# Kernel optimization log

Hardware: AMD Instinct MI355X
Metric: run time of the kernel (lower is better)

## Reference

```python
import jax, jax.numpy as jnp
import numpy as np
from jax import lax

BN_EPS = 1e-5


def _spatial_gate(x, w, g, b, m, v):
    # x: [N, C, H, W]; ChannelPool -> [N, 2, H, W]; 7x7 conv -> [N,1,H,W]; BN (eval); sigmoid gate
    comp = jnp.stack([jnp.max(x, axis=1), jnp.mean(x, axis=1)], axis=1)
    o = lax.conv_general_dilated(comp, w, (1, 1), [(3, 3), (3, 3)],
                                 dimension_numbers=('NCHW', 'OIHW', 'NCHW'))
    o = (o - m[None, :, None, None]) * lax.rsqrt(v + BN_EPS)[None, :, None, None] \
        * g[None, :, None, None] + b[None, :, None, None]
    s = jax.nn.sigmoid(o)
    return x * s


def _eca_sort(x, w_eca):
    # global avg pool -> sort channels desc -> 1D conv over sorted seq -> sigmoid -> unsort -> gate
    y = jnp.mean(x, axis=(2, 3))               # [N, C]
    order = jnp.argsort(-y, axis=1)            # descending sort indices
    rank = jnp.argsort(order, axis=1)          # inverse permutation
    ys = jnp.take_along_axis(y, order, axis=1)  # sorted descending
    k = w_eca.shape[-1]
    p = k // 2
    o = lax.conv_general_dilated(ys[:, None, :], w_eca, (1,), [(p, p)],
                                 dimension_numbers=('NCH', 'OIH', 'NCH'))[:, 0, :]
    sig = jax.nn.sigmoid(o)
    yr = jnp.take_along_axis(sig, rank, axis=1)  # reorder back per original index_select(rank)
    return x * yr[:, :, None, None]


def setup_inputs() -> dict:
    key = jax.random.key(0)
    ks = jax.random.split(key, 6)
    N, C, H, W = 32, 256, 56, 56
    inp = {
        'x': jax.random.normal(ks[0], (N, C, H, W), dtype=jnp.float32),
        'weight': jax.random.normal(ks[1], (1,), dtype=jnp.float32),
        'w_h': jax.random.normal(ks[2], (1, 2, 7, 7), dtype=jnp.float32) * 0.1,
        'g_h': jnp.ones((1,), jnp.float32), 'b_h': jnp.zeros((1,), jnp.float32),
        'm_h': jnp.zeros((1,), jnp.float32), 'v_h': jnp.ones((1,), jnp.float32),
        'w_w': jax.random.normal(ks[3], (1, 2, 7, 7), dtype=jnp.float32) * 0.1,
        'g_w': jnp.ones((1,), jnp.float32), 'b_w': jnp.zeros((1,), jnp.float32),
        'm_w': jnp.zeros((1,), jnp.float32), 'v_w': jnp.ones((1,), jnp.float32),
        'w_s': jax.random.normal(ks[4], (1, 2, 7, 7), dtype=jnp.float32) * 0.1,
        'g_s': jnp.ones((1,), jnp.float32), 'b_s': jnp.zeros((1,), jnp.float32),
        'm_s': jnp.zeros((1,), jnp.float32), 'v_s': jnp.ones((1,), jnp.float32),
        'w_eca': jax.random.normal(ks[5], (1, 1, 5), dtype=jnp.float32) * 0.3,
    }
    return inp


def reference(x, weight, w_h, g_h, b_h, m_h, v_h, w_w, g_w, b_w, m_w, v_w,
              w_s, g_s, b_s, m_s, v_s, w_eca):
    # branch 1: gate over H-as-channel (permute 0,2,1,3)
    xh = jnp.transpose(x, (0, 2, 1, 3))
    x11 = jnp.transpose(_spatial_gate(xh, w_h, g_h, b_h, m_h, v_h), (0, 2, 1, 3))
    # branch 2: gate over W-as-channel (permute 0,3,2,1)
    xw = jnp.transpose(x, (0, 3, 2, 1))
    x21 = jnp.transpose(_spatial_gate(xw, w_w, g_w, b_w, m_w, v_w), (0, 3, 2, 1))
    # branch 3: eca with sort/unsort
    x31 = _eca_sort(x, w_eca)
    # branch 4: plain spatial gate
    xo = _spatial_gate(x, w_s, g_s, b_s, m_s, v_s)
    return 0.23779 * xo + 0.24695 * x11 + 0.24365 * x21 + 0.27173 * x31
```

## Files before the change

### kernel.cpp

```cpp
#include <hip/hip_runtime.h>
#include <math.h>

#define N_ 32
#define C_ 256
#define H_ 56
#define W_ 56
#define HW_ (H_*W_)
#define HW4_ (HW_/4)
#define CHW_ (C_*HW_)
#define NHW_ (N_*HW_)
#define NCW_ (N_*C_*W_)
#define NHC_ (N_*H_*C_)
#define BN_EPS_ 1e-5f

#define TLD 60
#define PLANES_PER_BLK 8
#define NB_PL 1024
#define NB_CP 784

#define SM_BUF1 3360
#define SM_CPMX 6720
#define SM_CPSM (6720 + 224)
#define SM_TOT  (6720 + 448)

__global__ __launch_bounds__(256) void pools_k(
        const float* __restrict__ x,
        float* __restrict__ maxC, float* __restrict__ meanC,
        float* __restrict__ maxH, float* __restrict__ meanH,
        float* __restrict__ maxW, float* __restrict__ meanW,
        float* __restrict__ y) {
    __shared__ float smem[SM_TOT];
    int b = blockIdx.x;
    int tid = threadIdx.x;
    const float4* x4 = (const float4*)x;
    if (b < NB_PL) {
        float* buf0 = smem;
        float* buf1 = smem + SM_BUF1;
        float* cpmx = smem + SM_CPMX;
        float* cpsm = smem + SM_CPSM;
        int pb0 = b * PLANES_PER_BLK;
        float4 r0, r1, r2, r3;
        int row0 = tid / 14,          col0 = (tid % 14) * 4;
        int row1 = (tid + 256) / 14,  col1 = ((tid + 256) % 14) * 4;
        int row2 = (tid + 512) / 14,  col2 = ((tid + 512) % 14) * 4;
        int row3 = (tid + 768) / 14,  col3 = ((tid + 768) % 14) * 4;
        {
            size_t base = (size_t)pb0 * HW4_;
            r0 = x4[base + tid];
            r1 = x4[base + 256 + tid];
            r2 = x4[base + 512 + tid];
            if (tid < 16) r3 = x4[base + 768 + tid];
        }
        {
            float* d = buf0;
            *(float4*)&d[row0 * TLD + col0] = r0;
            *(float4*)&d[row1 * TLD + col1] = r1;
            *(float4*)&d[row2 * TLD + col2] = r2;
            if (tid < 16) *(float4*)&d[row3 * TLD + col3] = r3;
        }
        __syncthreads();
        for (int k = 0; k < PLANES_PER_BLK; ++k) {
            float* cur = (k & 1) ? buf1 : buf0;
            float* nxt = (k & 1) ? buf0 : buf1;
            int pb = pb0 + k;
            int n = pb >> 8, c = pb & 255;
            if (k < PLANES_PER_BLK - 1) {
                size_t base = (size_t)(pb + 1) * HW4_;
                r0 = x4[base + tid];
                r1 = x4[base + 256 + tid];
                r2 = x4[base + 512 + tid];
                if (tid < 16) r3 = x4[base + 768 + tid];
            }
            if (tid < 224) {
                int w = tid % 56, hq = tid / 56;
                const float* base = &cur[(hq * 14) * TLD + w];
                float mx = -INFINITY, sm = 0.f;
                #pragma unroll
                for (int hh = 0; hh < 14; ++hh) {
                    float v = base[hh * TLD];
                    mx = fmaxf(mx, v); sm += v;
                }
                cpmx[hq * 56 + w] = mx;
                cpsm[hq * 56 + w] = sm;
            }
            __syncthreads();
            float colsum = 0.f;
            if (tid < 56) {
                float mx = cpmx[tid], sm = cpsm[tid];
                #pragma unroll
                for (int j = 1; j < 4; ++j) {
                    mx = fmaxf(mx, cpmx[j * 56 + tid]);
                    sm += cpsm[j * 56 + tid];
                }
                int o = (n * C_ + c) * W_ + tid;
                maxH[o] = mx;
                meanH[o] = sm * (1.f / H_);
                colsum = sm;
            }
            if (tid < 64) {
                float t = colsum;
                #pragma unroll
                for (int off = 32; off >= 1; off >>= 1) t += __shfl_xor(t, off);
                if (tid == 0) y[n * C_ + c] = t * (1.f / HW_);
            }
            if (tid < 224) {
                int h = tid >> 2, kq = tid & 3;
                const float* base = &cur[h * TLD + kq * 14];
                float mx = -INFINITY, sm = 0.f;
                #pragma unroll
                for (int kk = 0; kk < 14; ++kk) {
                    float v = base[kk];
                    mx = fmaxf(mx, v); sm += v;
                }
                mx = fmaxf(mx, __shfl_xor(mx, 1)); sm += __shfl_xor(sm, 1);
                mx = fmaxf(mx, __shfl_xor(mx, 2)); sm += __shfl_xor(sm, 2);
                if (kq == 0) {
                    int o = (n * H_ + h) * C_ + c;
                    maxW[o] = mx;
                    meanW[o] = sm * (1.f / W_);
                }
            }
            if (k < PLANES_PER_BLK - 1) {
                *(float4*)&nxt[row0 * TLD + col0] = r0;
                *(float4*)&nxt[row1 * TLD + col1] = r1;
                *(float4*)&nxt[row2 * TLD + col2] = r2;
                if (tid < 16) *(float4*)&nxt[row3 * TLD + col3] = r3;
            }
            __syncthreads();
        }
    } else {
        float4* smx = (float4*)smem;
        float4* ssm = smx + 256;
        int bb = b - NB_PL;
        int g = tid >> 5, qi = tid & 31;
        int q = bb * 32 + qi;
        int n = q / HW4_;
        int hw4 = q - n * HW4_;
        size_t base = (size_t)n * (CHW_ / 4) + hw4 + (size_t)(g * 32) * HW4_;
        float4 mx = make_float4(-INFINITY, -INFINITY, -INFINITY, -INFINITY);
        float4 sm = make_float4(0.f, 0.f, 0.f, 0.f);
        #pragma unroll 16
        for (int i = 0; i < 32; ++i) {
            float4 v = x4[base + (size_t)i * HW4_];
            mx.x = fmaxf(mx.x, v.x); mx.y = fmaxf(mx.y, v.y);
            mx.z = fmaxf(mx.z, v.z); mx.w = fmaxf(mx.w, v.w);
            sm.x += v.x; sm.y += v.y; sm.z += v.z; sm.w += v.w;
        }
        smx[g * 32 + qi] = mx;
        ssm[g * 32 + qi] = sm;
        __syncthreads();
        if (tid < 32) {
            float4 m = smx[tid];
            #pragma unroll
            for (int j = 1; j < 8; ++j) {
                float4 v = smx[j * 32 + tid];
                m.x = fmaxf(m.x, v.x); m.y = fmaxf(m.y, v.y);
                m.z = fmaxf(m.z, v.z); m.w = fmaxf(m.w, v.w);
            }
            ((float4*)maxC)[bb * 32 + tid] = m;
        } else if (tid < 64) {
            int t2 = tid - 32;
            float4 s = ssm[t2];
            #pragma unroll
            for (int j = 1; j < 8; ++j) {
                float4 v = ssm[j * 32 + t2];
                s.x += v.x; s.y += v.y; s.z += v.z; s.w += v.w;
            }
            s.x *= (1.f / C_); s.y *= (1.f / C_); s.z *= (1.f / C_); s.w *= (1.f / C_);
            ((float4*)meanC)[bb * 32 + t2] = s;
        }
    }
}

template <int R, int Cc>
__device__ __forceinline__ void conv7_part(int t, const float* __restrict__ p0,
                                           const float* __restrict__ p1,
                                           const float* __restrict__ wt,
                                           float g, float bb, float m, float v,
                                           float* __restrict__ out) {
    const int per = R * Cc;
    int n = t / per;
    int r2 = t - n * per;
    int i = r2 / Cc, j = r2 - i * Cc;
    const float* b0 = p0 + (size_t)n * per;
    const float* b1 = p1 + (size_t)n * per;
    float acc = 0.f;
    #pragma unroll
    for (int ki = 0; ki < 7; ++ki) {
        int ii = i + ki - 3;
        if (ii < 0 || ii >= R) continue;
        #pragma unroll
        for (int kj = 0; kj < 7; ++kj) {
            int jj = j + kj - 3;
            if (jj < 0 || jj >= Cc) continue;
            int idx = ii * Cc + jj;
            acc += b0[idx] * wt[ki * 7 + kj] + b1[idx] * wt[49 + ki * 7 + kj];
        }
    }
    float o = (acc - m) * rsqrtf(v + BN_EPS_) * g + bb;
    out[t] = 1.f / (1.f + expf(-o));
}

#define NB_SS (NHW_ / 256)
#define NB_SH (NCW_ / 256)
#define NB_SW (NHC_ / 256)

__global__ __launch_bounds__(256) void conv_eca_k(
        const float* __restrict__ maxC, const float* __restrict__ meanC,
        const float* __restrict__ maxH, const float* __restrict__ meanH,
        const float* __restrict__ maxW, const float* __restrict__ meanW,
        const float* __restrict__ w_s, const float* __restrict__ g_s,
        const float* __restrict__ b_s, const float* __restrict__ m_s,
        const float* __restrict__ v_s,
        const float* __restrict__ w_h, const float* __restrict__ g_h,
        const float* __restrict__ b_h, const float* __restrict__ m_h,
        const float* __restrict__ v_h,
        const float* __restrict__ w_w, const float* __restrict__ g_w,
        const float* __restrict__ b_w, const float* __restrict__ m_w,
        const float* __restrict__ v_w,
        const float* __restrict__ y, const float* __restrict__ w_eca,
        float* __restrict__ s_s, float* __restrict__ s_h, float* __restrict__ s_w,
        float* __restrict__ gate) {
    __shared__ float sv[C_];
    __shared__ int si[C_];
    int b = blockIdx.x;
    int tid = threadIdx.x;
    if (b < NB_SS) {
        conv7_part<H_, W_>(b * 256 + tid, maxC, meanC, w_s, g_s[0], b_s[0], m_s[0],
                           v_s[0], s_s);
    } else if (b < NB_SS + NB_SH) {
        conv7_part<C_, W_>((b - NB_SS) * 256 + tid, maxH, meanH, w_h, g_h[0], b_h[0],
                           m_h[0], v_h[0], s_h);
    } else if (b < NB_SS + NB_SH + NB_SW) {
        conv7_part<H_, C_>((b - NB_SS - NB_SH) * 256 + tid, maxW, meanW, w_w, g_w[0],
                           b_w[0], m_w[0], v_w[0], s_w);
    } else {
        int n = b - (NB_SS + NB_SH + NB_SW);
        sv[tid] = y[n * C_ + tid];
        si[tid] = tid;
        __syncthreads();
        for (int k = 2; k <= C_; k <<= 1) {
            for (int j = k >> 1; j > 0; j >>= 1) {
                int ixj = tid ^ j;
                if (ixj > tid) {
                    float v1 = sv[tid], v2 = sv[ixj];
                    int i1 = si[tid], i2 = si[ixj];
                    bool before = (v1 > v2) || (v1 == v2 && i1 < i2);
                    bool dir = ((tid & k) == 0);
                    if (dir ? !before : before) {
                        sv[tid] = v2; sv[ixj] = v1;
                        si[tid] = i2; si[ixj] = i1;
                    }
                }
                __syncthreads();
            }
        }
        float o = 0.f;
        #pragma unroll
        for (int j = 0; j < 5; ++j) {
            int p = tid + j - 2;
            if (p >= 0 && p < C_) o += sv[p] * w_eca[j];
        }
        gate[n * C_ + si[tid]] = 1.f / (1.f + expf(-o));
    }
}

__global__ __launch_bounds__(256) void apply_k(
        const float* __restrict__ x, const float* __restrict__ s_s,
        const float* __restrict__ s_h, const float* __restrict__ s_w,
        const float* __restrict__ gate, float* __restrict__ out) {
    int t0 = blockIdx.x * 512 + threadIdx.x;
    #pragma unroll
    for (int r = 0; r < 2; ++r) {
        int t = t0 + r * 256;
        int f = t * 4;
        int n = f / CHW_;
        int rem = f - n * CHW_;
        int c = rem / HW_;
        int hw = rem - c * HW_;
        int h = hw / W_;
        int w = hw - h * W_;
        float4 xv = ((const float4*)x)[t];
        float4 s4 = *(const float4*)(s_s + (size_t)n * HW_ + hw);
        float4 h4 = *(const float4*)(s_h + ((size_t)n * C_ + c) * W_ + w);
        float sw = s_w[((size_t)n * H_ + h) * C_ + c];
        float ge = gate[n * C_ + c];
        float base = 0.24365f * sw + 0.27173f * ge;
        float4 o;
        o.x = xv.x * (0.23779f * s4.x + 0.24695f * h4.x + base);
        o.y = xv.y * (0.23779f * s4.y + 0.24695f * h4.y + base);
        o.z = xv.z * (0.23779f * s4.z + 0.24695f * h4.z + base);
        o.w = xv.w * (0.23779f * s4.w + 0.24695f * h4.w + base);
        ((float4*)out)[t] = o;
    }
}

extern "C" void kernel_launch(void* const* d_in, const int* in_sizes, int n_in,
                              void* d_out, int out_size, void* d_ws, size_t ws_size,
                              hipStream_t stream) {
    const float* x     = (const float*)d_in[0];
    const float* w_h   = (const float*)d_in[2];
    const float* g_h   = (const float*)d_in[3];
    const float* b_h   = (const float*)d_in[4];
    const float* m_h   = (const float*)d_in[5];
    const float* v_h   = (const float*)d_in[6];
    const float* w_w   = (const float*)d_in[7];
    const float* g_w   = (const float*)d_in[8];
    const float* b_w   = (const float*)d_in[9];
    const float* m_w   = (const float*)d_in[10];
    const float* v_w   = (const float*)d_in[11];
    const float* w_s   = (const float*)d_in[12];
    const float* g_s   = (const float*)d_in[13];
    const float* b_s   = (const float*)d_in[14];
    const float* m_s   = (const float*)d_in[15];
    const float* v_s   = (const float*)d_in[16];
    const float* w_eca = (const float*)d_in[17];
    float* out = (float*)d_out;

    float* ws    = (float*)d_ws;
    float* maxC  = ws;
    float* meanC = maxC  + NHW_;
    float* maxH  = meanC + NHW_;
    float* meanH = maxH  + NCW_;
    float* maxW  = meanH + NCW_;
    float* meanW = maxW  + NHC_;
    float* s_s   = meanW + NHC_;
    float* s_h   = s_s   + NHW_;
    float* s_w   = s_h   + NCW_;
    float* yv    = s_w   + NHC_;
    float* gate  = yv    + N_ * C_;

    pools_k<<<NB_PL + NB_CP, 256, 0, stream>>>(x, maxC, meanC, maxH, meanH,
                                               maxW, meanW, yv);

    int conv_blocks = NB_SS + NB_SH + NB_SW + N_;
    conv_eca_k<<<conv_blocks, 256, 0, stream>>>(maxC, meanC, maxH, meanH, maxW, meanW,
                                                w_s, g_s, b_s, m_s, v_s,
                                                w_h, g_h, b_h, m_h, v_h,
                                                w_w, g_w, b_w, m_w, v_w,
                                                yv, w_eca, s_s, s_h, s_w, gate);

    apply_k<<<(N_ * CHW_ / 4) / 512, 256, 0, stream>>>(x, s_s, s_h, s_w, gate, out);
}
```

Measured before the change: 110.6 us.

## Fuse channel pooling into plane-pooling pass with partial reductions plus finalize kernel

The channel max/mean pool previously re-read all of x in separate blocks of the pools kernel. Now each plane-pooling block also accumulates per-pixel max/sum across its 8 channel planes from registers it already loads, writes partials, and a small new kernel reduces 32 partials per pixel. This removes a second full read of x at the cost of writing and reading partial buffers (about 2x NB_PL*HW floats) and an extra kernel launch.

```diff
diff --git a/kernel.cpp b/kernel.cpp
--- a/kernel.cpp
+++ b/kernel.cpp
@@ -9,6 +9,7 @@
 #define HW4_ (HW_/4)
 #define CHW_ (C_*HW_)
 #define NHW_ (N_*HW_)
+#define NHW4_ (NHW_/4)
 #define NCW_ (N_*C_*W_)
 #define NHC_ (N_*H_*C_)
 #define BN_EPS_ 1e-5f
@@ -16,160 +17,157 @@
 #define TLD 60
 #define PLANES_PER_BLK 8
 #define NB_PL 1024
-#define NB_CP 784
 
 #define SM_BUF1 3360
 #define SM_CPMX 6720
 #define SM_CPSM (6720 + 224)
 #define SM_TOT  (6720 + 448)
 
+#define F4MAX(a,b) do { (a).x=fmaxf((a).x,(b).x); (a).y=fmaxf((a).y,(b).y); \
+                        (a).z=fmaxf((a).z,(b).z); (a).w=fmaxf((a).w,(b).w); } while(0)
+#define F4ADD(a,b) do { (a).x+=(b).x; (a).y+=(b).y; (a).z+=(b).z; (a).w+=(b).w; } while(0)
+
 __global__ __launch_bounds__(256) void pools_k(
         const float* __restrict__ x,
-        float* __restrict__ maxC, float* __restrict__ meanC,
         float* __restrict__ maxH, float* __restrict__ meanH,
         float* __restrict__ maxW, float* __restrict__ meanW,
+        float* __restrict__ pmx, float* __restrict__ psm,
         float* __restrict__ y) {
     __shared__ float smem[SM_TOT];
     int b = blockIdx.x;
     int tid = threadIdx.x;
     const float4* x4 = (const float4*)x;
-    if (b < NB_PL) {
-        float* buf0 = smem;
-        float* buf1 = smem + SM_BUF1;
-        float* cpmx = smem + SM_CPMX;
-        float* cpsm = smem + SM_CPSM;
-        int pb0 = b * PLANES_PER_BLK;
-        float4 r0, r1, r2, r3;
-        int row0 = tid / 14,          col0 = (tid % 14) * 4;
-        int row1 = (tid + 256) / 14,  col1 = ((tid + 256) % 14) * 4;
-        int row2 = (tid + 512) / 14,  col2 = ((tid + 512) % 14) * 4;
-        int row3 = (tid + 768) / 14,  col3 = ((tid + 768) % 14) * 4;
-        {
-            size_t base = (size_t)pb0 * HW4_;
+    float* buf0 = smem;
+    float* buf1 = smem + SM_BUF1;
+    float* cpmx = smem + SM_CPMX;
+    float* cpsm = smem + SM_CPSM;
+    int pb0 = b * PLANES_PER_BLK;
+    float4 r0, r1, r2, r3;
+    int row0 = tid / 14,          col0 = (tid % 14) * 4;
+    int row1 = (tid + 256) / 14,  col1 = ((tid + 256) % 14) * 4;
+    int row2 = (tid + 512) / 14,  col2 = ((tid + 512) % 14) * 4;
+    int row3 = (tid + 768) / 14,  col3 = ((tid + 768) % 14) * 4;
+    float4 amx0, amx1, amx2, amx3, asm0, asm1, asm2, asm3;
+    amx0 = amx1 = amx2 = amx3 = make_float4(-INFINITY, -INFINITY, -INFINITY, -INFINITY);
+    asm0 = asm1 = asm2 = asm3 = make_float4(0.f, 0.f, 0.f, 0.f);
+    {
+        size_t base = (size_t)pb0 * HW4_;
+        r0 = x4[base + tid];
+        r1 = x4[base + 256 + tid];
+        r2 = x4[base + 512 + tid];
+        if (tid < 16) r3 = x4[base + 768 + tid];
+        F4MAX(amx0, r0); F4ADD(asm0, r0);
+        F4MAX(amx1, r1); F4ADD(asm1, r1);
+        F4MAX(amx2, r2); F4ADD(asm2, r2);
+        if (tid < 16) { F4MAX(amx3, r3); F4ADD(asm3, r3); }
+        *(float4*)&buf0[row0 * TLD + col0] = r0;
+        *(float4*)&buf0[row1 * TLD + col1] = r1;
+        *(float4*)&buf0[row2 * TLD + col2] = r2;
+        if (tid < 16) *(float4*)&buf0[row3 * TLD + col3] = r3;
+    }
+    __syncthreads();
+    for (int k = 0; k < PLANES_PER_BLK; ++k) {
+        float* cur = (k & 1) ? buf1 : buf0;
+        float* nxt = (k & 1) ? buf0 : buf1;
+        int pb = pb0 + k;
+        int n = pb >> 8, c = pb & 255;
+        if (k < PLANES_PER_BLK - 1) {
+            size_t base = (size_t)(pb + 1) * HW4_;
             r0 = x4[base + tid];
             r1 = x4[base + 256 + tid];
             r2 = x4[base + 512 + tid];
             if (tid < 16) r3 = x4[base + 768 + tid];
         }
-        {
-            float* d = buf0;
-            *(float4*)&d[row0 * TLD + col0] = r0;
-            *(float4*)&d[row1 * TLD + col1] = r1;
-            *(float4*)&d[row2 * TLD + col2] = r2;
-            if (tid < 16) *(float4*)&d[row3 * TLD + col3] = r3;
+        if (tid < 224) {
+            int w = tid % 56, hq = tid / 56;
+            const float* base = &cur[(hq * 14) * TLD + w];
+            float mx = -INFINITY, sm = 0.f;
+            #pragma unroll
+            for (int hh = 0; hh < 14; ++hh) {
+                float v = base[hh * TLD];
+                mx = fmaxf(mx, v); sm += v;
+            }
+            cpmx[hq * 56 + w] = mx;
+            cpsm[hq * 56 + w] = sm;
         }
         __syncthreads();
-        for (int k = 0; k < PLANES_PER_BLK; ++k) {
-            float* cur = (k & 1) ? buf1 : buf0;
-            float* nxt = (k & 1) ? buf0 : buf1;
-            int pb = pb0 + k;
-            int n = pb >> 8, c = pb & 255;
-            if (k < PLANES_PER_BLK - 1) {
-                size_t base = (size_t)(pb + 1) * HW4_;
-                r0 = x4[base + tid];
-                r1 = x4[base + 256 + tid];
-                r2 = x4[base + 512 + tid];
-                if (tid < 16) r3 = x4[base + 768 + tid];
-            }
-            if (tid < 224) {
-                int w = tid % 56, hq = tid / 56;
-                const float* base = &cur[(hq * 14) * TLD + w];
-                float mx = -INFINITY, sm = 0.f;
-                #pragma unroll
-                for (int hh = 0; hh < 14; ++hh) {
-                    float v = base[hh * TLD];
-                    mx = fmaxf(mx, v); sm += v;
-                }
-                cpmx[hq * 56 + w] = mx;
-                cpsm[hq * 56 + w] = sm;
-            }
-            __syncthreads();
-            float colsum = 0.f;
-            if (tid < 56) {
-                float mx = cpmx[tid], sm = cpsm[tid];
-                #pragma unroll
-                for (int j = 1; j < 4; ++j) {
-                    mx = fmaxf(mx, cpmx[j * 56 + tid]);
-                    sm += cpsm[j * 56 + tid];
-                }
-                int o = (n * C_ + c) * W_ + tid;
-                maxH[o] = mx;
-                meanH[o] = sm * (1.f / H_);
-                colsum = sm;
-            }
-            if (tid < 64) {
-                float t = colsum;
-                #pragma unroll
-                for (int off = 32; off >= 1; off >>= 1) t += __shfl_xor(t, off);
-                if (tid == 0) y[n * C_ + c] = t * (1.f / HW_);
-            }
-            if (tid < 224) {
-                int h = tid >> 2, kq = tid & 3;
-                const float* base = &cur[h * TLD + kq * 14];
-                float mx = -INFINITY, sm = 0.f;
-                #pragma unroll
-                for (int kk = 0; kk < 14; ++kk) {
-                    float v = base[kk];
-                    mx = fmaxf(mx, v); sm += v;
-                }
-                mx = fmaxf(mx, __shfl_xor(mx, 1)); sm += __shfl_xor(sm, 1);
-                mx = fmaxf(mx, __shfl_xor(mx, 2)); sm += __shfl_xor(sm, 2);
-                if (kq == 0) {
-                    int o = (n * H_ + h) * C_ + c;
-                    maxW[o] = mx;
-                    meanW[o] = sm * (1.f / W_);
-                }
-            }
-            if (k < PLANES_PER_BLK - 1) {
-                *(float4*)&nxt[row0 * TLD + col0] = r0;
-                *(float4*)&nxt[row1 * TLD + col1] = r1;
-                *(float4*)&nxt[row2 * TLD + col2] = r2;
-                if (tid < 16) *(float4*)&nxt[row3 * TLD + col3] = r3;
-            }
-            __syncthreads();
-        }
-    } else {
-        float4* smx = (float4*)smem;
-        float4* ssm = smx + 256;
-        int bb = b - NB_PL;
-        int g = tid >> 5, qi = tid & 31;
-        int q = bb * 32 + qi;
-        int n = q / HW4_;
-        int hw4 = q - n * HW4_;
-        size_t base = (size_t)n * (CHW_ / 4) + hw4 + (size_t)(g * 32) * HW4_;
-        float4 mx = make_float4(-INFINITY, -INFINITY, -INFINITY, -INFINITY);
-        float4 sm = make_float4(0.f, 0.f, 0.f, 0.f);
-        #pragma unroll 16
-        for (int i = 0; i < 32; ++i) {
-            float4 v = x4[base + (size_t)i * HW4_];
-            mx.x = fmaxf(mx.x, v.x); mx.y = fmaxf(mx.y, v.y);
-            mx.z = fmaxf(mx.z, v.z); mx.w = fmaxf(mx.w, v.w);
-            sm.x += v.x; sm.y += v.y; sm.z += v.z; sm.w += v.w;
-        }
-        smx[g * 32 + qi] = mx;
-        ssm[g * 32 + qi] = sm;
+        float colsum = 0.f;
+        if (tid < 56) {
+            float mx = cpmx[tid], sm = cpsm[tid];
+            #pragma unroll
+            for (int j = 1; j < 4; ++j) {
+                mx = fmaxf(mx, cpmx[j * 56 + tid]);
+                sm += cpsm[j * 56 + tid];
+            }
+            int o = (n * C_ + c) * W_ + tid;
+            maxH[o] = mx;
+            meanH[o] = sm * (1.f / H_);
+            colsum = sm;
+        }
+        if (tid < 64) {
+            float t = colsum;
+            #pragma unroll
+            for (int off = 32; off >= 1; off >>= 1) t += __shfl_xor(t, off);
+            if (tid == 0) y[n * C_ + c] = t * (1.f / HW_);
+        }
+        if (tid < 224) {
+            int h = tid >> 2, kq = tid & 3;
+            const float* base = &cur[h * TLD + kq * 14];
+            float mx = -INFINITY, sm = 0.f;
+            #pragma unroll
+            for (int kk = 0; kk < 14; ++kk) {
+                float v = base[kk];
+                mx = fmaxf(mx, v); sm += v;
+            }
+            mx = fmaxf(mx, __shfl_xor(mx, 1)); sm += __shfl_xor(sm, 1);
+            mx = fmaxf(mx, __shfl_xor(mx, 2)); sm += __shfl_xor(sm, 2);
+            if (kq == 0) {
+                int o = (n * H_ + h) * C_ + c;
+                maxW[o] = mx;
+                meanW[o] = sm * (1.f / W_);
+            }
+        }
+        if (k < PLANES_PER_BLK - 1) {
+            F4MAX(amx0, r0); F4ADD(asm0, r0);
+            F4MAX(amx1, r1); F4ADD(asm1, r1);
+            F4MAX(amx2, r2); F4ADD(asm2, r2);
+            if (tid < 16) { F4MAX(amx3, r3); F4ADD(asm3, r3); }
+            *(float4*)&nxt[row0 * TLD + col0] = r0;
+            *(float4*)&nxt[row1 * TLD + col1] = r1;
+            *(float4*)&nxt[row2 * TLD + col2] = r2;
+            if (tid < 16) *(float4*)&nxt[row3 * TLD + col3] = r3;
+        }
         __syncthreads();
-        if (tid < 32) {
-            float4 m = smx[tid];
-            #pragma unroll
-            for (int j = 1; j < 8; ++j) {
-                float4 v = smx[j * 32 + tid];
-                m.x = fmaxf(m.x, v.x); m.y = fmaxf(m.y, v.y);
-                m.z = fmaxf(m.z, v.z); m.w = fmaxf(m.w, v.w);
-            }
-            ((float4*)maxC)[bb * 32 + tid] = m;
-        } else if (tid < 64) {
-            int t2 = tid - 32;
-            float4 s = ssm[t2];
-            #pragma unroll
-            for (int j = 1; j < 8; ++j) {
-                float4 v = ssm[j * 32 + t2];
-                s.x += v.x; s.y += v.y; s.z += v.z; s.w += v.w;
-            }
-            s.x *= (1.f / C_); s.y *= (1.f / C_); s.z *= (1.f / C_); s.w *= (1.f / C_);
-            ((float4*)meanC)[bb * 32 + t2] = s;
-        }
-    }
+    }
+    {
+        float4* PM = (float4*)pmx + (size_t)b * HW4_;
+        float4* PS = (float4*)psm + (size_t)b * HW4_;
+        PM[tid] = amx0;        PS[tid] = asm0;
+        PM[tid + 256] = amx1;  PS[tid + 256] = asm1;
+        PM[tid + 512] = amx2;  PS[tid + 512] = asm2;
+        if (tid < 16) { PM[tid + 768] = amx3; PS[tid + 768] = asm3; }
+    }
+}
+
+__global__ __launch_bounds__(256) void cpool_final_k(
+        const float* __restrict__ pmx, const float* __restrict__ psm,
+        float* __restrict__ maxC, float* __restrict__ meanC) {
+    int t = blockIdx.x * 256 + threadIdx.x;
+    int n = t / HW4_, hw4 = t - n * HW4_;
+    const float4* PM = (const float4*)pmx + (size_t)(n * 32) * HW4_ + hw4;
+    const float4* PS = (const float4*)psm + (size_t)(n * 32) * HW4_ + hw4;
+    float4 mx = make_float4(-INFINITY, -INFINITY, -INFINITY, -INFINITY);
+    float4 sm = make_float4(0.f, 0.f, 0.f, 0.f);
+    #pragma unroll 8
+    for (int g = 0; g < 32; ++g) {
+        float4 v = PM[(size_t)g * HW4_];
+        float4 s = PS[(size_t)g * HW4_];
+        F4MAX(mx, v);
+        F4ADD(sm, s);
+    }
+    sm.x *= (1.f / C_); sm.y *= (1.f / C_); sm.z *= (1.f / C_); sm.w *= (1.f / C_);
+    ((float4*)maxC)[t] = mx;
+    ((float4*)meanC)[t] = sm;
 }
 
 template <int R, int Cc>
@@ -329,9 +327,12 @@
     float* s_w   = s_h   + NCW_;
     float* yv    = s_w   + NHC_;
     float* gate  = yv    + N_ * C_;
-
-    pools_k<<<NB_PL + NB_CP, 256, 0, stream>>>(x, maxC, meanC, maxH, meanH,
-                                               maxW, meanW, yv);
+    float* pmx   = gate  + N_ * C_;
+    float* psm   = pmx   + NB_PL * HW_;
+
+    pools_k<<<NB_PL, 256, 0, stream>>>(x, maxH, meanH, maxW, meanW, pmx, psm, yv);
+
+    cpool_final_k<<<NHW4_ / 256, 256, 0, stream>>>(pmx, psm, maxC, meanC);
 
     int conv_blocks = NB_SS + NB_SH + NB_SW + N_;
     conv_eca_k<<<conv_blocks, 256, 0, stream>>>(maxC, meanC, maxH, meanH, maxW, meanW,
```

New measurement: 104.8 us. -5.2%, faster.
